# Kernel optimization log

Hardware: AMD Instinct MI355X
Metric: run time of the kernel (lower is better)

## Reference

```python
import jax, jax.numpy as jnp
import numpy as np

K = 8            # number of iterative top-k relaxation steps (init arg k)
TAU = 1.0        # softmax temperature (global `tau` in the original source)
EPS = float(np.finfo(np.float32).tiny)  # self.eps in the original


def setup_inputs() -> dict:
    key = jax.random.key(0)
    # [B, H, M, N] as required by the unsqueeze(-2).repeat([1,1,1,k,1]) in forward
    scores = jax.random.normal(key, (8, 8, 256, 1024), dtype=jnp.float32)
    return {"scores": scores, "hard": 0}


def _soft_topk(scores):
    """k-step iterative softmax relaxation. Returns (khot [...,N], khot_M [...,K,N])."""
    zero = jnp.zeros_like(scores)

    def step(carry, _):
        s, onehot, khot = carry
        khot_mask = jnp.maximum(1.0 - onehot, EPS)
        s = s + jnp.log(khot_mask)
        onehot = jax.nn.softmax(s / TAU, axis=-1)
        return (s, onehot, khot + onehot), onehot

    (_, _, khot), oh_stack = jax.lax.scan(step, (scores, zero, zero), None, length=K)
    khot_M = jnp.moveaxis(oh_stack, 0, -2)  # [K, B, H, M, N] -> [B, H, M, K, N]
    return khot, khot_M


def reference(scores, hard):
    khot, khot_M = _soft_topk(scores)
    if hard:
        n = scores.shape[-1]
        _, ind = jax.lax.top_k(khot, K)                       # [..., K]
        res = jnp.sum(jax.nn.one_hot(ind, n, dtype=khot.dtype), axis=-2)
        res_M = jax.nn.one_hot(jnp.argmax(khot_M, axis=-1), n, dtype=khot.dtype)
    else:
        res, res_M = khot, khot_M
    return (res, res_M)
```

## Files before the change

### kernel.cpp

```cpp
#include <hip/hip_runtime.h>

namespace {

constexpr int KSTEPS = 8;
constexpr int N      = 1024;
constexpr int ROWS   = 8 * 8 * 256;
constexpr int EPT    = N / 64;
constexpr float EPS  = 1.17549435082228751e-38f;

__global__ __launch_bounds__(256) void soft_topk_kernel(
    const float* __restrict__ scores,
    float* __restrict__ out_khot,
    float* __restrict__ out_khotM)
{
    const int wave = threadIdx.x >> 6;
    const int lane = threadIdx.x & 63;
    const int row  = blockIdx.x * 4 + wave;

    const float4* __restrict__ src =
        reinterpret_cast<const float4*>(scores + (size_t)row * N);

    float s[EPT], oh[EPT], kh[EPT];

    #pragma unroll
    for (int c = 0; c < 4; ++c) {
        float4 v = src[c * 64 + lane];
        s[c*4+0] = v.x; s[c*4+1] = v.y; s[c*4+2] = v.z; s[c*4+3] = v.w;
    }
    #pragma unroll
    for (int i = 0; i < EPT; ++i) { oh[i] = 0.0f; kh[i] = 0.0f; }

    float4* __restrict__ dstM =
        reinterpret_cast<float4*>(out_khotM + (size_t)row * (KSTEPS * N));

    #pragma unroll
    for (int step = 0; step < KSTEPS; ++step) {
        if (step > 0) {
            #pragma unroll
            for (int i = 0; i < EPT; ++i) {
                float mask = fmaxf(1.0f - oh[i], EPS);
                s[i] += __logf(mask);
            }
        }

        float m = s[0];
        #pragma unroll
        for (int i = 1; i < EPT; ++i) m = fmaxf(m, s[i]);
        #pragma unroll
        for (int off = 32; off >= 1; off >>= 1)
            m = fmaxf(m, __shfl_xor(m, off, 64));

        float sum = 0.0f;
        #pragma unroll
        for (int i = 0; i < EPT; ++i) {
            oh[i] = __expf(s[i] - m);
            sum += oh[i];
        }
        #pragma unroll
        for (int off = 32; off >= 1; off >>= 1)
            sum += __shfl_xor(sum, off, 64);

        const float rinv = 1.0f / sum;
        #pragma unroll
        for (int i = 0; i < EPT; ++i) {
            oh[i] *= rinv;
            kh[i] += oh[i];
        }

        #pragma unroll
        for (int c = 0; c < 4; ++c) {
            float4 v = make_float4(oh[c*4+0], oh[c*4+1], oh[c*4+2], oh[c*4+3]);
            dstM[step * (N / 4) + c * 64 + lane] = v;
        }
    }

    float4* __restrict__ dstK =
        reinterpret_cast<float4*>(out_khot + (size_t)row * N);
    #pragma unroll
    for (int c = 0; c < 4; ++c) {
        float4 v = make_float4(kh[c*4+0], kh[c*4+1], kh[c*4+2], kh[c*4+3]);
        dstK[c * 64 + lane] = v;
    }
}

}

extern "C" void kernel_launch(void* const* d_in, const int* in_sizes, int n_in,
                              void* d_out, int out_size, void* d_ws, size_t ws_size,
                              hipStream_t stream) {
    const float* scores = (const float*)d_in[0];
    float* out_khot  = (float*)d_out;
    float* out_khotM = (float*)d_out + (size_t)ROWS * N;

    soft_topk_kernel<<<dim3(ROWS / 4), dim3(256), 0, stream>>>(
        scores, out_khot, out_khotM);
}
```

Measured before the change: 133.5 us.

## Replace per-step log/softmax with multiplicative mask update and nontemporal I/O

```diff
diff --git a/kernel.cpp b/kernel.cpp
--- a/kernel.cpp
+++ b/kernel.cpp
@@ -1,6 +1,8 @@
 #include <hip/hip_runtime.h>
 
 namespace {
+
+typedef float f32x4 __attribute__((ext_vector_type(4)));
 
 constexpr int KSTEPS = 8;
 constexpr int N      = 1024;
@@ -17,69 +19,71 @@
     const int lane = threadIdx.x & 63;
     const int row  = blockIdx.x * 4 + wave;
 
-    const float4* __restrict__ src =
-        reinterpret_cast<const float4*>(scores + (size_t)row * N);
+    const f32x4* __restrict__ src =
+        reinterpret_cast<const f32x4*>(scores + (size_t)row * N);
+    f32x4* __restrict__ dstM =
+        reinterpret_cast<f32x4*>(out_khotM + (size_t)row * (KSTEPS * N));
+    f32x4* __restrict__ dstK =
+        reinterpret_cast<f32x4*>(out_khot + (size_t)row * N);
 
-    float s[EPT], oh[EPT], kh[EPT];
+    float u[EPT], kh[EPT];
 
     #pragma unroll
     for (int c = 0; c < 4; ++c) {
-        float4 v = src[c * 64 + lane];
-        s[c*4+0] = v.x; s[c*4+1] = v.y; s[c*4+2] = v.z; s[c*4+3] = v.w;
+        f32x4 v = __builtin_nontemporal_load(&src[c * 64 + lane]);
+        u[c*4+0] = v[0]; u[c*4+1] = v[1]; u[c*4+2] = v[2]; u[c*4+3] = v[3];
+    }
+
+    float m = u[0];
+    #pragma unroll
+    for (int i = 1; i < EPT; ++i) m = fmaxf(m, u[i]);
+    #pragma unroll
+    for (int off = 32; off >= 1; off >>= 1)
+        m = fmaxf(m, __shfl_xor(m, off, 64));
+
+    float sum = 0.0f;
+    #pragma unroll
+    for (int i = 0; i < EPT; ++i) {
+        u[i] = __expf(u[i] - m);
+        sum += u[i];
     }
     #pragma unroll
-    for (int i = 0; i < EPT; ++i) { oh[i] = 0.0f; kh[i] = 0.0f; }
+    for (int off = 32; off >= 1; off >>= 1)
+        sum += __shfl_xor(sum, off, 64);
 
-    float4* __restrict__ dstM =
-        reinterpret_cast<float4*>(out_khotM + (size_t)row * (KSTEPS * N));
+    #pragma unroll
+    for (int i = 0; i < EPT; ++i) kh[i] = 0.0f;
 
     #pragma unroll
     for (int step = 0; step < KSTEPS; ++step) {
-        if (step > 0) {
+        const float rinv = __builtin_amdgcn_rcpf(sum);
+        float sumn = 0.0f;
+        #pragma unroll
+        for (int c = 0; c < 4; ++c) {
+            f32x4 v;
             #pragma unroll
-            for (int i = 0; i < EPT; ++i) {
-                float mask = fmaxf(1.0f - oh[i], EPS);
-                s[i] += __logf(mask);
+            for (int j = 0; j < 4; ++j) {
+                const int i = c*4 + j;
+                const float ohv = u[i] * rinv;
+                v[j] = ohv;
+                kh[i] += ohv;
+                const float un = u[i] * fmaxf(1.0f - ohv, EPS);
+                u[i] = un;
+                sumn += un;
             }
-        }
-
-        float m = s[0];
-        #pragma unroll
-        for (int i = 1; i < EPT; ++i) m = fmaxf(m, s[i]);
-        #pragma unroll
-        for (int off = 32; off >= 1; off >>= 1)
-            m = fmaxf(m, __shfl_xor(m, off, 64));
-
-        float sum = 0.0f;
-        #pragma unroll
-        for (int i = 0; i < EPT; ++i) {
-            oh[i] = __expf(s[i] - m);
-            sum += oh[i];
+            __builtin_nontemporal_store(v, &dstM[step * (N/4) + c * 64 + lane]);
         }
         #pragma unroll
         for (int off = 32; off >= 1; off >>= 1)
-            sum += __shfl_xor(sum, off, 64);
-
-        const float rinv = 1.0f / sum;
-        #pragma unroll
-        for (int i = 0; i < EPT; ++i) {
-            oh[i] *= rinv;
-            kh[i] += oh[i];
-        }
-
-        #pragma unroll
-        for (int c = 0; c < 4; ++c) {
-            float4 v = make_float4(oh[c*4+0], oh[c*4+1], oh[c*4+2], oh[c*4+3]);
-            dstM[step * (N / 4) + c * 64 + lane] = v;
-        }
+            sumn += __shfl_xor(sumn, off, 64);
+        sum = sumn;
     }
 
-    float4* __restrict__ dstK =
-        reinterpret_cast<float4*>(out_khot + (size_t)row * N);
     #pragma unroll
     for (int c = 0; c < 4; ++c) {
-        float4 v = make_float4(kh[c*4+0], kh[c*4+1], kh[c*4+2], kh[c*4+3]);
-        dstK[c * 64 + lane] = v;
+        f32x4 v;
+        v[0] = kh[c*4+0]; v[1] = kh[c*4+1]; v[2] = kh[c*4+2]; v[3] = kh[c*4+3];
+        __builtin_nontemporal_store(v, &dstK[c * 64 + lane]);
     }
 }
 
```

Result: faster. 130.5 us (-2.2%).
